# Performance work log

Hardware: AMD Instinct MI355X
Metric: run time of the kernel (lower is better)

The kernel has to match this reference:

```python
import jax, jax.numpy as jnp
import numpy as np

B, L, D_IN, D_EXP, N_EXP = 4, 2048, 1024, 1024, 8


def setup_inputs() -> dict:
    key = jax.random.key(0)
    ks = jax.random.split(key, 5)
    s_in = 1.0 / np.sqrt(D_IN)
    x = jax.random.normal(ks[0], (B, L, D_IN), dtype=jnp.float32)
    # per-expert Dense kernels/biases: (n, d_in, d_exp), (n, d_exp)
    We = jax.random.normal(ks[1], (N_EXP, D_IN, D_EXP), dtype=jnp.float32) * s_in
    be = jnp.zeros((N_EXP, D_EXP), dtype=jnp.float32)
    # gating Dense: (d_in, n), (n)
    Wg = jax.random.normal(ks[2], (D_IN, N_EXP), dtype=jnp.float32) * s_in
    bg = jnp.zeros((N_EXP,), dtype=jnp.float32)
    return {"x": x, "We": We, "be": be, "Wg": Wg, "bg": bg}


def reference(x, We, be, Wg, bg):
    # expert outputs: (b, l, n, d_exp) = relu(x @ We[n] + be[n])
    h = jax.nn.relu(jnp.einsum('bld,ndk->blnk', x, We) + be[None, None, :, :])
    # gate: softmax over experts, (b, l, n)
    gate = jax.nn.softmax(jnp.einsum('bld,dn->bln', x, Wg) + bg, axis=-1)
    # gated weighted sum over experts -> (b, l, d_exp)
    return jnp.einsum('bln,blnk->blk', gate, h)
```

## Files before the change

kernel.cpp:

```cpp
#include <hip/hip_runtime.h>
#include <hip/hip_bf16.h>
#include <stdint.h>

#define M_TOT 8192
#define DIN   1024
#define DEXP  1024
#define NEXP  8

#define BM 256
#define BN 128
#define BK 32
#define NT 128
#define KPP 32
#define SLOT_E 16384
#define EXPSZ (DEXP * DIN)

typedef __attribute__((ext_vector_type(8))) short bf16x8;
typedef __attribute__((ext_vector_type(16))) float f32x16;
typedef __attribute__((ext_vector_type(8))) unsigned short us8;

typedef __attribute__((address_space(1))) void* as1vp;
typedef __attribute__((address_space(3))) void* as3vp;

__device__ __forceinline__ unsigned short f2bf(float f) {
    union { float f; unsigned u; } v; v.f = f;
    return (unsigned short)((v.u + 0x7fffu + ((v.u >> 16) & 1u)) >> 16);
}

__device__ __forceinline__ void gl_lds16(const unsigned short* g, unsigned short* l) {
    __builtin_amdgcn_global_load_lds((as1vp)g, (as3vp)l, 16, 0, 0);
}

#define MFMA32(va, vb, vc) __builtin_amdgcn_mfma_f32_32x32x16_bf16(va, vb, vc, 0, 0, 0)

__global__ __launch_bounds__(256) void cvt_x_k(const float* __restrict__ in,
                                               unsigned short* __restrict__ out, int n8) {
    int i = blockIdx.x * 256 + threadIdx.x;
    int stride = gridDim.x * 256;
    for (; i < n8; i += stride) {
        const float4* p = (const float4*)in + (size_t)i * 2;
        float4 a = p[0], b = p[1];
        us8 o;
        o[0] = f2bf(a.x); o[1] = f2bf(a.y); o[2] = f2bf(a.z); o[3] = f2bf(a.w);
        o[4] = f2bf(b.x); o[5] = f2bf(b.y); o[6] = f2bf(b.z); o[7] = f2bf(b.w);
        *(us8*)(out + (size_t)i * 8) = o;
    }
}

__global__ __launch_bounds__(256) void cvt_w_k(const float* __restrict__ We,
                                               unsigned short* __restrict__ Wt) {
    __shared__ float tile[64][65];
    int n  = blockIdx.z;
    int k0 = blockIdx.y * 64;
    int j0 = blockIdx.x * 64;
    int t  = threadIdx.x;
    int tr = t >> 6, tc = t & 63;
    const float* src = We + (size_t)n * DIN * DEXP;
    #pragma unroll
    for (int rr = 0; rr < 16; ++rr) {
        int r = rr * 4 + tr;
        tile[r][tc] = src[(size_t)(k0 + r) * DEXP + j0 + tc];
    }
    __syncthreads();
    unsigned short* dst = Wt + (size_t)n * DEXP * DIN;
    #pragma unroll
    for (int rr = 0; rr < 16; ++rr) {
        int r = rr * 4 + tr;
        dst[(size_t)(j0 + r) * DIN + k0 + tc] = f2bf(tile[tc][r]);
    }
}

__global__ __launch_bounds__(256) void gate_k(const float* __restrict__ x,
                                              const float* __restrict__ Wg,
                                              const float* __restrict__ bg,
                                              float* __restrict__ gate) {
    __shared__ float wgt[NEXP][DIN];
    int t = threadIdx.x;
    for (int idx = t; idx < DIN * NEXP; idx += 256)
        wgt[idx & 7][idx >> 3] = Wg[idx];
    __syncthreads();
    int wid = t >> 6, lane = t & 63;
    for (int m = blockIdx.x * 4 + wid; m < M_TOT; m += gridDim.x * 4) {
        const float* xr = x + (size_t)m * DIN;
        float acc[NEXP];
        #pragma unroll
        for (int n = 0; n < NEXP; ++n) acc[n] = 0.f;
        for (int i = 0; i < DIN / 64; ++i) {
            int d = i * 64 + lane;
            float xv = xr[d];
            #pragma unroll
            for (int n = 0; n < NEXP; ++n) acc[n] = fmaf(xv, wgt[n][d], acc[n]);
        }
        #pragma unroll
        for (int n = 0; n < NEXP; ++n) {
            #pragma unroll
            for (int off = 32; off; off >>= 1) acc[n] += __shfl_xor(acc[n], off);
            acc[n] += bg[n];
        }
        float mx = acc[0];
        #pragma unroll
        for (int n = 1; n < NEXP; ++n) mx = fmaxf(mx, acc[n]);
        float s = 0.f, e[NEXP];
        #pragma unroll
        for (int n = 0; n < NEXP; ++n) { e[n] = __expf(acc[n] - mx); s += e[n]; }
        float inv = 1.f / s;
        if (lane < NEXP) gate[(size_t)m * NEXP + lane] = e[lane] * inv;
    }
}

__global__ __launch_bounds__(512, 2) void moe_k(const unsigned short* __restrict__ Xb,
                                                const unsigned short* __restrict__ Wt,
                                                const float* __restrict__ gate,
                                                const float* __restrict__ be,
                                                float* __restrict__ out) {
    __shared__ __align__(16) unsigned short lds[4 * SLOT_E];
    __shared__ float gateL[BM * NEXP];
    __shared__ float biasL[NEXP * BN];

    const int t    = threadIdx.x;
    const int lane = t & 63;
    const int wv   = t >> 6;
    const int wm   = wv >> 1;
    const int wn   = wv & 1;
    const int l31  = lane & 31;
    const int lhi  = lane >> 5;

    const int b    = blockIdx.x;
    const int lg   = (b & 7) * 32 + (b >> 3);
    const int brow = (lg >> 3) * BM;
    const int bcol = (lg & 7) * BN;

    const int sA = (t >> 2) * DIN + ((((t & 3) - (t >> 3)) & 3) * 8);
    const unsigned short* gA = Xb + (size_t)brow * DIN;
    const unsigned short* gB = Wt + (size_t)bcol * DIN;

    const int kc0 = ((lhi + (l31 >> 1)) & 3) * 8;
    const int kc1 = kc0 ^ 16;
    const int aOff0 = (wm * 64 + l31) * 32 + kc0;
    const int aOff1 = (wm * 64 + l31) * 32 + kc1;
    const int bOff0 = 8192 + (wn * 64 + l31) * 32 + kc0;
    const int bOff1 = 8192 + (wn * 64 + l31) * 32 + kc1;

#define STAGE_A(sl_, k0_) do { \
    const unsigned short* g_ = gA + (k0_) + sA; \
    unsigned short* d_ = (unsigned short*)lds + (sl_) * SLOT_E + t * 8; \
    gl_lds16(g_, d_); gl_lds16(g_ + 128 * DIN, d_ + 4096); } while (0)
#define STAGE_B0(sl_, e_, k0_) do { \
    gl_lds16(gB + (size_t)(e_) * EXPSZ + (k0_) + sA, \
             (unsigned short*)lds + (sl_) * SLOT_E + 8192 + t * 8); } while (0)
#define STAGE_B1(sl_, e_, k0_) do { \
    gl_lds16(gB + (size_t)(e_) * EXPSZ + (k0_) + sA, \
             (unsigned short*)lds + (sl_) * SLOT_E + 12288 + t * 8); } while (0)

#define RD_B0(L_) do { \
    b0[0][0] = *(const bf16x8*)((L_) + bOff0); \
    b0[0][1] = *(const bf16x8*)((L_) + bOff1); \
    b0[1][0] = *(const bf16x8*)((L_) + bOff0 + 1024); \
    b0[1][1] = *(const bf16x8*)((L_) + bOff1 + 1024); } while (0)
#define RD_A(L_) do { \
    a[0][0] = *(const bf16x8*)((L_) + aOff0); \
    a[0][1] = *(const bf16x8*)((L_) + aOff1); \
    a[1][0] = *(const bf16x8*)((L_) + aOff0 + 1024); \
    a[1][1] = *(const bf16x8*)((L_) + aOff1 + 1024); } while (0)
#define RD_B1(L_) do { \
    b1[0][0] = *(const bf16x8*)((L_) + bOff0 + 4096); \
    b1[0][1] = *(const bf16x8*)((L_) + bOff1 + 4096); \
    b1[1][0] = *(const bf16x8*)((L_) + bOff0 + 5120); \
    b1[1][1] = *(const bf16x8*)((L_) + bOff1 + 5120); } while (0)

    f32x16 acc_e0[2][2] = {};
    f32x16 acc_e1[2][2] = {};
    f32x16 acc_o[2][2]  = {};
    bf16x8 a[2][2], b0[2][2], b1[2][2];

    {
        const float* gp = gate + (size_t)brow * NEXP;
        ((float4*)gateL)[t] = ((const float4*)gp)[t];
        if (t < 256)
            ((float4*)biasL)[t] =
                *(const float4*)(be + (size_t)(t >> 5) * DEXP + bcol + (t & 31) * 4);
    }
    STAGE_A(0, 0);  STAGE_B0(0, 0, 0);  STAGE_B1(0, 1, 0);
    STAGE_A(1, 32); STAGE_B0(1, 0, 32); STAGE_B1(1, 1, 32);
    STAGE_A(2, 64); STAGE_B0(2, 0, 64); STAGE_B1(2, 1, 64);
    asm volatile("s_waitcnt vmcnt(4)" ::: "memory");
    asm volatile("s_waitcnt lgkmcnt(0)" ::: "memory");
    __builtin_amdgcn_s_barrier();
    RD_B0(lds); RD_A(lds);
    __builtin_amdgcn_sched_barrier(0);
    RD_B1(lds);
    __builtin_amdgcn_sched_barrier(0);

    for (int T = 0; T < NT; ++T) {
        asm volatile("s_waitcnt lgkmcnt(4)" ::: "memory");
        __builtin_amdgcn_sched_barrier(0);
        __builtin_amdgcn_s_setprio(1);
        #pragma unroll
        for (int mf = 0; mf < 2; ++mf)
            #pragma unroll
            for (int nf = 0; nf < 2; ++nf) {
                acc_e0[mf][nf] = MFMA32(a[mf][0], b0[nf][0], acc_e0[mf][nf]);
                acc_e0[mf][nf] = MFMA32(a[mf][1], b0[nf][1], acc_e0[mf][nf]);
            }
        __builtin_amdgcn_s_setprio(0);

        if (T < NT - 1) {
            const unsigned short* L1 = lds + ((T + 1) & 3) * SLOT_E;
            RD_B0(L1);
            asm volatile("s_waitcnt lgkmcnt(4)" ::: "memory");
        } else {
            asm volatile("s_waitcnt lgkmcnt(0)" ::: "memory");
        }
        __builtin_amdgcn_sched_barrier(0);
        __builtin_amdgcn_s_setprio(1);
        #pragma unroll
        for (int mf = 0; mf < 2; ++mf)
            #pragma unroll
            for (int nf = 0; nf < 2; ++nf) {
                acc_e1[mf][nf] = MFMA32(a[mf][0], b1[nf][0], acc_e1[mf][nf]);
                acc_e1[mf][nf] = MFMA32(a[mf][1], b1[nf][1], acc_e1[mf][nf]);
            }
        __builtin_amdgcn_s_setprio(0);

        if ((T & (KPP - 1)) == (KPP - 1)) {
            const int e0 = (T >> 5) * 2, e1 = e0 + 1;
            float bi0[2], bi1[2];
            #pragma unroll
            for (int nf = 0; nf < 2; ++nf) {
                bi0[nf] = biasL[e0 * BN + wn * 64 + nf * 32 + l31];
                bi1[nf] = biasL[e1 * BN + wn * 64 + nf * 32 + l31];
            }
            #pragma unroll
            for (int mf = 0; mf < 2; ++mf) {
                #pragma unroll
                for (int reg = 0; reg < 16; ++reg) {
                    const int rl = wm * 64 + mf * 32 + (reg & 3) + 8 * (reg >> 2) + 4 * lhi;
                    const float g0 = gateL[rl * NEXP + e0];
                    const float g1 = gateL[rl * NEXP + e1];
                    #pragma unroll
                    for (int nf = 0; nf < 2; ++nf) {
                        acc_o[mf][nf][reg] += g0 * fmaxf(acc_e0[mf][nf][reg] + bi0[nf], 0.f)
                                            + g1 * fmaxf(acc_e1[mf][nf][reg] + bi1[nf], 0.f);
                    }
                }
            }
            #pragma unroll
            for (int mf = 0; mf < 2; ++mf)
                #pragma unroll
                for (int nf = 0; nf < 2; ++nf) {
                    acc_e0[mf][nf] = (f32x16){};
                    acc_e1[mf][nf] = (f32x16){};
                }
        }

        if (T < NT - 1) {
            const unsigned short* L1 = lds + ((T + 1) & 3) * SLOT_E;
            RD_A(L1);
            __builtin_amdgcn_sched_barrier(0);
            RD_B1(L1);
            __builtin_amdgcn_sched_barrier(0);
        }

        if (T < NT - 3) {
            const int s3 = (T + 3) & 3;
            const int e3 = ((T + 3) >> 5) * 2;
            const int k3 = ((T + 3) & (KPP - 1)) * BK;
            STAGE_A(s3, k3); STAGE_B0(s3, e3, k3); STAGE_B1(s3, e3 + 1, k3);
            asm volatile("s_waitcnt vmcnt(4)" ::: "memory");
        } else {
            asm volatile("s_waitcnt vmcnt(0)" ::: "memory");
        }
        __builtin_amdgcn_s_barrier();
    }

    #pragma unroll
    for (int mf = 0; mf < 2; ++mf) {
        #pragma unroll
        for (int reg = 0; reg < 16; ++reg) {
            const int rl = wm * 64 + mf * 32 + (reg & 3) + 8 * (reg >> 2) + 4 * lhi;
            float* op = out + (size_t)(brow + rl) * DEXP + bcol + wn * 64 + l31;
            #pragma unroll
            for (int nf = 0; nf < 2; ++nf) op[nf * 32] = acc_o[mf][nf][reg];
        }
    }
#undef STAGE_A
#undef STAGE_B0
#undef STAGE_B1
#undef RD_A
#undef RD_B0
#undef RD_B1
}

extern "C" void kernel_launch(void* const* d_in, const int* in_sizes, int n_in,
                              void* d_out, int out_size, void* d_ws, size_t ws_size,
                              hipStream_t stream) {
    const float* x  = (const float*)d_in[0];
    const float* We = (const float*)d_in[1];
    const float* be = (const float*)d_in[2];
    const float* Wg = (const float*)d_in[3];
    const float* bg = (const float*)d_in[4];
    float* out = (float*)d_out;

    unsigned short* Xb = (unsigned short*)d_ws;
    unsigned short* Wt = Xb + (size_t)M_TOT * DIN;
    float* gate = (float*)(Wt + (size_t)NEXP * DEXP * DIN);

    hipLaunchKernelGGL(cvt_x_k, dim3(2048), dim3(256), 0, stream, x, Xb, M_TOT * DIN / 8);
    hipLaunchKernelGGL(cvt_w_k, dim3(16, 16, 8), dim3(256), 0, stream, We, Wt);
    hipLaunchKernelGGL(gate_k, dim3(512), dim3(256), 0, stream, x, Wg, bg, gate);
    hipLaunchKernelGGL(moe_k, dim3((M_TOT / BM) * (DEXP / BN)), dim3(512), 0, stream,
                       Xb, Wt, gate, be, out);
}
```

Measured before the change: 159.8 us.

## Fuse x bf16 conversion into gate kernel and double-buffer A fragments in MoE loop

Removes the separate x-to-bf16 kernel and does the conversion inside the gating kernel, which already reads each row of x. This saves one launch and one full read of x. In the main MFMA loop, A fragments are now double-buffered in registers (aX/aY) and the loop is unrolled by two. The next A and B0 fragments are read from LDS right after the first MFMA group rather than after the epilogue, to overlap LDS reads with compute. This costs more VGPRs and changes the lgkmcnt wait thresholds, which could hurt occupancy or scheduling.

Result: slower. 351.5 us (+119.9%).

```diff
diff --git a/kernel.cpp b/kernel.cpp
--- a/kernel.cpp
+++ b/kernel.cpp
@@ -32,20 +32,6 @@
 }
 
 #define MFMA32(va, vb, vc) __builtin_amdgcn_mfma_f32_32x32x16_bf16(va, vb, vc, 0, 0, 0)
-
-__global__ __launch_bounds__(256) void cvt_x_k(const float* __restrict__ in,
-                                               unsigned short* __restrict__ out, int n8) {
-    int i = blockIdx.x * 256 + threadIdx.x;
-    int stride = gridDim.x * 256;
-    for (; i < n8; i += stride) {
-        const float4* p = (const float4*)in + (size_t)i * 2;
-        float4 a = p[0], b = p[1];
-        us8 o;
-        o[0] = f2bf(a.x); o[1] = f2bf(a.y); o[2] = f2bf(a.z); o[3] = f2bf(a.w);
-        o[4] = f2bf(b.x); o[5] = f2bf(b.y); o[6] = f2bf(b.z); o[7] = f2bf(b.w);
-        *(us8*)(out + (size_t)i * 8) = o;
-    }
-}
 
 __global__ __launch_bounds__(256) void cvt_w_k(const float* __restrict__ We,
                                                unsigned short* __restrict__ Wt) {
@@ -70,10 +56,11 @@
     }
 }
 
-__global__ __launch_bounds__(256) void gate_k(const float* __restrict__ x,
-                                              const float* __restrict__ Wg,
-                                              const float* __restrict__ bg,
-                                              float* __restrict__ gate) {
+__global__ __launch_bounds__(256) void gatex_k(const float* __restrict__ x,
+                                               const float* __restrict__ Wg,
+                                               const float* __restrict__ bg,
+                                               float* __restrict__ gate,
+                                               unsigned short* __restrict__ Xb) {
     __shared__ float wgt[NEXP][DIN];
     int t = threadIdx.x;
     for (int idx = t; idx < DIN * NEXP; idx += 256)
@@ -82,6 +69,17 @@
     int wid = t >> 6, lane = t & 63;
     for (int m = blockIdx.x * 4 + wid; m < M_TOT; m += gridDim.x * 4) {
         const float* xr = x + (size_t)m * DIN;
+        unsigned short* xb = Xb + (size_t)m * DIN;
+        #pragma unroll
+        for (int p = 0; p < 2; ++p) {
+            int d = p * 512 + lane * 8;
+            float4 v0 = *(const float4*)(xr + d);
+            float4 v1 = *(const float4*)(xr + d + 4);
+            us8 o;
+            o[0] = f2bf(v0.x); o[1] = f2bf(v0.y); o[2] = f2bf(v0.z); o[3] = f2bf(v0.w);
+            o[4] = f2bf(v1.x); o[5] = f2bf(v1.y); o[6] = f2bf(v1.z); o[7] = f2bf(v1.w);
+            *(us8*)(xb + d) = o;
+        }
         float acc[NEXP];
         #pragma unroll
         for (int n = 0; n < NEXP; ++n) acc[n] = 0.f;
@@ -157,11 +155,11 @@
     b0[0][1] = *(const bf16x8*)((L_) + bOff1); \
     b0[1][0] = *(const bf16x8*)((L_) + bOff0 + 1024); \
     b0[1][1] = *(const bf16x8*)((L_) + bOff1 + 1024); } while (0)
-#define RD_A(L_) do { \
-    a[0][0] = *(const bf16x8*)((L_) + aOff0); \
-    a[0][1] = *(const bf16x8*)((L_) + aOff1); \
-    a[1][0] = *(const bf16x8*)((L_) + aOff0 + 1024); \
-    a[1][1] = *(const bf16x8*)((L_) + aOff1 + 1024); } while (0)
+#define RD_AS(S_, L_) do { \
+    S_[0][0] = *(const bf16x8*)((L_) + aOff0); \
+    S_[0][1] = *(const bf16x8*)((L_) + aOff1); \
+    S_[1][0] = *(const bf16x8*)((L_) + aOff0 + 1024); \
+    S_[1][1] = *(const bf16x8*)((L_) + aOff1 + 1024); } while (0)
 #define RD_B1(L_) do { \
     b1[0][0] = *(const bf16x8*)((L_) + bOff0 + 4096); \
     b1[0][1] = *(const bf16x8*)((L_) + bOff1 + 4096); \
@@ -171,7 +169,7 @@
     f32x16 acc_e0[2][2] = {};
     f32x16 acc_e1[2][2] = {};
     f32x16 acc_o[2][2]  = {};
-    bf16x8 a[2][2], b0[2][2], b1[2][2];
+    bf16x8 aX[2][2], aY[2][2], b0[2][2], b1[2][2];
 
     {
         const float* gp = gate + (size_t)brow * NEXP;
@@ -186,91 +184,93 @@
     asm volatile("s_waitcnt vmcnt(4)" ::: "memory");
     asm volatile("s_waitcnt lgkmcnt(0)" ::: "memory");
     __builtin_amdgcn_s_barrier();
-    RD_B0(lds); RD_A(lds);
+    RD_B0(lds);
+    __builtin_amdgcn_sched_barrier(0);
+    RD_AS(aX, lds);
     __builtin_amdgcn_sched_barrier(0);
     RD_B1(lds);
     __builtin_amdgcn_sched_barrier(0);
 
-    for (int T = 0; T < NT; ++T) {
-        asm volatile("s_waitcnt lgkmcnt(4)" ::: "memory");
-        __builtin_amdgcn_sched_barrier(0);
-        __builtin_amdgcn_s_setprio(1);
-        #pragma unroll
-        for (int mf = 0; mf < 2; ++mf)
-            #pragma unroll
-            for (int nf = 0; nf < 2; ++nf) {
-                acc_e0[mf][nf] = MFMA32(a[mf][0], b0[nf][0], acc_e0[mf][nf]);
-                acc_e0[mf][nf] = MFMA32(a[mf][1], b0[nf][1], acc_e0[mf][nf]);
-            }
-        __builtin_amdgcn_s_setprio(0);
-
-        if (T < NT - 1) {
-            const unsigned short* L1 = lds + ((T + 1) & 3) * SLOT_E;
-            RD_B0(L1);
-            asm volatile("s_waitcnt lgkmcnt(4)" ::: "memory");
-        } else {
-            asm volatile("s_waitcnt lgkmcnt(0)" ::: "memory");
-        }
-        __builtin_amdgcn_sched_barrier(0);
-        __builtin_amdgcn_s_setprio(1);
-        #pragma unroll
-        for (int mf = 0; mf < 2; ++mf)
-            #pragma unroll
-            for (int nf = 0; nf < 2; ++nf) {
-                acc_e1[mf][nf] = MFMA32(a[mf][0], b1[nf][0], acc_e1[mf][nf]);
-                acc_e1[mf][nf] = MFMA32(a[mf][1], b1[nf][1], acc_e1[mf][nf]);
-            }
-        __builtin_amdgcn_s_setprio(0);
-
-        if ((T & (KPP - 1)) == (KPP - 1)) {
-            const int e0 = (T >> 5) * 2, e1 = e0 + 1;
-            float bi0[2], bi1[2];
-            #pragma unroll
-            for (int nf = 0; nf < 2; ++nf) {
-                bi0[nf] = biasL[e0 * BN + wn * 64 + nf * 32 + l31];
-                bi1[nf] = biasL[e1 * BN + wn * 64 + nf * 32 + l31];
-            }
-            #pragma unroll
-            for (int mf = 0; mf < 2; ++mf) {
-                #pragma unroll
-                for (int reg = 0; reg < 16; ++reg) {
-                    const int rl = wm * 64 + mf * 32 + (reg & 3) + 8 * (reg >> 2) + 4 * lhi;
-                    const float g0 = gateL[rl * NEXP + e0];
-                    const float g1 = gateL[rl * NEXP + e1];
-                    #pragma unroll
-                    for (int nf = 0; nf < 2; ++nf) {
-                        acc_o[mf][nf][reg] += g0 * fmaxf(acc_e0[mf][nf][reg] + bi0[nf], 0.f)
-                                            + g1 * fmaxf(acc_e1[mf][nf][reg] + bi1[nf], 0.f);
-                    }
-                }
-            }
-            #pragma unroll
-            for (int mf = 0; mf < 2; ++mf)
-                #pragma unroll
-                for (int nf = 0; nf < 2; ++nf) {
-                    acc_e0[mf][nf] = (f32x16){};
-                    acc_e1[mf][nf] = (f32x16){};
-                }
-        }
-
-        if (T < NT - 1) {
-            const unsigned short* L1 = lds + ((T + 1) & 3) * SLOT_E;
-            RD_A(L1);
-            __builtin_amdgcn_sched_barrier(0);
-            RD_B1(L1);
-            __builtin_amdgcn_sched_barrier(0);
-        }
-
-        if (T < NT - 3) {
-            const int s3 = (T + 3) & 3;
-            const int e3 = ((T + 3) >> 5) * 2;
-            const int k3 = ((T + 3) & (KPP - 1)) * BK;
-            STAGE_A(s3, k3); STAGE_B0(s3, e3, k3); STAGE_B1(s3, e3 + 1, k3);
-            asm volatile("s_waitcnt vmcnt(4)" ::: "memory");
-        } else {
-            asm volatile("s_waitcnt vmcnt(0)" ::: "memory");
-        }
-        __builtin_amdgcn_s_barrier();
+#define EPILOGUE(pg_) do { \
+    const int e0_ = (pg_) * 2, e1_ = e0_ + 1; \
+    float bi0[2], bi1[2]; \
+    _Pragma("unroll") \
+    for (int nf = 0; nf < 2; ++nf) { \
+        bi0[nf] = biasL[e0_ * BN + wn * 64 + nf * 32 + l31]; \
+        bi1[nf] = biasL[e1_ * BN + wn * 64 + nf * 32 + l31]; \
+    } \
+    _Pragma("unroll") \
+    for (int mf = 0; mf < 2; ++mf) { \
+        _Pragma("unroll") \
+        for (int reg = 0; reg < 16; ++reg) { \
+            const int rl_ = wm * 64 + mf * 32 + (reg & 3) + 8 * (reg >> 2) + 4 * lhi; \
+            const float g0_ = gateL[rl_ * NEXP + e0_]; \
+            const float g1_ = gateL[rl_ * NEXP + e1_]; \
+            _Pragma("unroll") \
+            for (int nf = 0; nf < 2; ++nf) { \
+                acc_o[mf][nf][reg] += g0_ * fmaxf(acc_e0[mf][nf][reg] + bi0[nf], 0.f) \
+                                    + g1_ * fmaxf(acc_e1[mf][nf][reg] + bi1[nf], 0.f); \
+            } \
+        } \
+    } \
+    _Pragma("unroll") \
+    for (int mf = 0; mf < 2; ++mf) \
+        _Pragma("unroll") \
+        for (int nf = 0; nf < 2; ++nf) { \
+            acc_e0[mf][nf] = (f32x16){}; \
+            acc_e1[mf][nf] = (f32x16){}; \
+        } } while (0)
+
+#define ITER(T_, AC, AN, DO_EPI) do { \
+    const unsigned short* L1_ = lds + (((T_) + 1) & 3) * SLOT_E; \
+    asm volatile("s_waitcnt lgkmcnt(4)" ::: "memory"); \
+    __builtin_amdgcn_sched_barrier(0); \
+    __builtin_amdgcn_s_setprio(1); \
+    _Pragma("unroll") \
+    for (int mf = 0; mf < 2; ++mf) \
+        _Pragma("unroll") \
+        for (int nf = 0; nf < 2; ++nf) { \
+            acc_e0[mf][nf] = MFMA32(AC[mf][0], b0[nf][0], acc_e0[mf][nf]); \
+            acc_e0[mf][nf] = MFMA32(AC[mf][1], b0[nf][1], acc_e0[mf][nf]); \
+        } \
+    __builtin_amdgcn_s_setprio(0); \
+    __builtin_amdgcn_sched_barrier(0); \
+    if ((T_) < NT - 1) { \
+        RD_B0(L1_); \
+        __builtin_amdgcn_sched_barrier(0); \
+        RD_AS(AN, L1_); \
+        __builtin_amdgcn_sched_barrier(0); \
+        asm volatile("s_waitcnt lgkmcnt(8)" ::: "memory"); \
+    } else { \
+        asm volatile("s_waitcnt lgkmcnt(0)" ::: "memory"); \
+    } \
+    __builtin_amdgcn_sched_barrier(0); \
+    __builtin_amdgcn_s_setprio(1); \
+    _Pragma("unroll") \
+    for (int mf = 0; mf < 2; ++mf) \
+        _Pragma("unroll") \
+        for (int nf = 0; nf < 2; ++nf) { \
+            acc_e1[mf][nf] = MFMA32(AC[mf][0], b1[nf][0], acc_e1[mf][nf]); \
+            acc_e1[mf][nf] = MFMA32(AC[mf][1], b1[nf][1], acc_e1[mf][nf]); \
+        } \
+    __builtin_amdgcn_s_setprio(0); \
+    __builtin_amdgcn_sched_barrier(0); \
+    if ((T_) < NT - 1) { RD_B1(L1_); __builtin_amdgcn_sched_barrier(0); } \
+    if (DO_EPI && (((T_) & (KPP - 1)) == (KPP - 1))) EPILOGUE((T_) >> 5); \
+    if ((T_) < NT - 3) { \
+        const int s3_ = ((T_) + 3) & 3; \
+        const int e3_ = (((T_) + 3) >> 5) * 2; \
+        const int k3_ = (((T_) + 3) & (KPP - 1)) * BK; \
+        STAGE_A(s3_, k3_); STAGE_B0(s3_, e3_, k3_); STAGE_B1(s3_, e3_ + 1, k3_); \
+        asm volatile("s_waitcnt vmcnt(4)" ::: "memory"); \
+    } else { \
+        asm volatile("s_waitcnt vmcnt(0)" ::: "memory"); \
+    } \
+    __builtin_amdgcn_s_barrier(); } while (0)
+
+    for (int T = 0; T < NT; T += 2) {
+        ITER(T,     aX, aY, 0);
+        ITER(T + 1, aY, aX, 1);
     }
 
     #pragma unroll
@@ -286,9 +286,11 @@
 #undef STAGE_A
 #undef STAGE_B0
 #undef STAGE_B1
-#undef RD_A
+#undef RD_AS
 #undef RD_B0
 #undef RD_B1
+#undef ITER
+#undef EPILOGUE
 }
 
 extern "C" void kernel_launch(void* const* d_in, const int* in_sizes, int n_in,
@@ -305,9 +307,8 @@
     unsigned short* Wt = Xb + (size_t)M_TOT * DIN;
     float* gate = (float*)(Wt + (size_t)NEXP * DEXP * DIN);
 
-    hipLaunchKernelGGL(cvt_x_k, dim3(2048), dim3(256), 0, stream, x, Xb, M_TOT * DIN / 8);
     hipLaunchKernelGGL(cvt_w_k, dim3(16, 16, 8), dim3(256), 0, stream, We, Wt);
-    hipLaunchKernelGGL(gate_k, dim3(512), dim3(256), 0, stream, x, Wg, bg, gate);
+    hipLaunchKernelGGL(gatex_k, dim3(512), dim3(256), 0, stream, x, Wg, bg, gate, Xb);
     hipLaunchKernelGGL(moe_k, dim3((M_TOT / BM) * (DEXP / BN)), dim3(512), 0, stream,
                        Xb, Wt, gate, be, out);
 }
```

## Shrink MoE GEMM tile to 128x128 with 3-stage LDS ring and fuse x conversion into gating

Applied to the files above, without the earlier changes.

Fuses the fp32-to-bf16 conversion of x into the gating kernel, so x is read once for both jobs and one launch is dropped. The main MoE GEMM tile shrinks from 256x128 with 512 threads to 128x128 with 256 threads. The LDS ring drops from 4 slots to 3, with the slot index and vmcnt waits adjusted to match. The grid doubles, which should give more blocks per CU and better wave balance, at the cost of lower arithmetic intensity per block and more weight re-reads.

After: 180.5 us. 1.13x slower.

```diff
diff --git a/kernel.cpp b/kernel.cpp
--- a/kernel.cpp
+++ b/kernel.cpp
@@ -7,12 +7,12 @@
 #define DEXP  1024
 #define NEXP  8
 
-#define BM 256
+#define BM 128
 #define BN 128
 #define BK 32
 #define NT 128
 #define KPP 32
-#define SLOT_E 16384
+#define SLOT_E 12288
 #define EXPSZ (DEXP * DIN)
 
 typedef __attribute__((ext_vector_type(8))) short bf16x8;
@@ -32,20 +32,6 @@
 }
 
 #define MFMA32(va, vb, vc) __builtin_amdgcn_mfma_f32_32x32x16_bf16(va, vb, vc, 0, 0, 0)
-
-__global__ __launch_bounds__(256) void cvt_x_k(const float* __restrict__ in,
-                                               unsigned short* __restrict__ out, int n8) {
-    int i = blockIdx.x * 256 + threadIdx.x;
-    int stride = gridDim.x * 256;
-    for (; i < n8; i += stride) {
-        const float4* p = (const float4*)in + (size_t)i * 2;
-        float4 a = p[0], b = p[1];
-        us8 o;
-        o[0] = f2bf(a.x); o[1] = f2bf(a.y); o[2] = f2bf(a.z); o[3] = f2bf(a.w);
-        o[4] = f2bf(b.x); o[5] = f2bf(b.y); o[6] = f2bf(b.z); o[7] = f2bf(b.w);
-        *(us8*)(out + (size_t)i * 8) = o;
-    }
-}
 
 __global__ __launch_bounds__(256) void cvt_w_k(const float* __restrict__ We,
                                                unsigned short* __restrict__ Wt) {
@@ -70,10 +56,11 @@
     }
 }
 
-__global__ __launch_bounds__(256) void gate_k(const float* __restrict__ x,
-                                              const float* __restrict__ Wg,
-                                              const float* __restrict__ bg,
-                                              float* __restrict__ gate) {
+__global__ __launch_bounds__(256) void gatex_k(const float* __restrict__ x,
+                                               const float* __restrict__ Wg,
+                                               const float* __restrict__ bg,
+                                               float* __restrict__ gate,
+                                               unsigned short* __restrict__ Xb) {
     __shared__ float wgt[NEXP][DIN];
     int t = threadIdx.x;
     for (int idx = t; idx < DIN * NEXP; idx += 256)
@@ -82,6 +69,17 @@
     int wid = t >> 6, lane = t & 63;
     for (int m = blockIdx.x * 4 + wid; m < M_TOT; m += gridDim.x * 4) {
         const float* xr = x + (size_t)m * DIN;
+        unsigned short* xb = Xb + (size_t)m * DIN;
+        #pragma unroll
+        for (int p = 0; p < 2; ++p) {
+            int d = p * 512 + lane * 8;
+            float4 v0 = *(const float4*)(xr + d);
+            float4 v1 = *(const float4*)(xr + d + 4);
+            us8 o;
+            o[0] = f2bf(v0.x); o[1] = f2bf(v0.y); o[2] = f2bf(v0.z); o[3] = f2bf(v0.w);
+            o[4] = f2bf(v1.x); o[5] = f2bf(v1.y); o[6] = f2bf(v1.z); o[7] = f2bf(v1.w);
+            *(us8*)(xb + d) = o;
+        }
         float acc[NEXP];
         #pragma unroll
         for (int n = 0; n < NEXP; ++n) acc[n] = 0.f;
@@ -108,12 +106,12 @@
     }
 }
 
-__global__ __launch_bounds__(512, 2) void moe_k(const unsigned short* __restrict__ Xb,
+__global__ __launch_bounds__(256, 2) void moe_k(const unsigned short* __restrict__ Xb,
                                                 const unsigned short* __restrict__ Wt,
                                                 const float* __restrict__ gate,
                                                 const float* __restrict__ be,
                                                 float* __restrict__ out) {
-    __shared__ __align__(16) unsigned short lds[4 * SLOT_E];
+    __shared__ __align__(16) unsigned short lds[3 * SLOT_E];
     __shared__ float gateL[BM * NEXP];
     __shared__ float biasL[NEXP * BN];
 
@@ -126,7 +124,7 @@
     const int lhi  = lane >> 5;
 
     const int b    = blockIdx.x;
-    const int lg   = (b & 7) * 32 + (b >> 3);
+    const int lg   = (b & 7) * 64 + (b >> 3);
     const int brow = (lg >> 3) * BM;
     const int bcol = (lg & 7) * BN;
 
@@ -138,19 +136,21 @@
     const int kc1 = kc0 ^ 16;
     const int aOff0 = (wm * 64 + l31) * 32 + kc0;
     const int aOff1 = (wm * 64 + l31) * 32 + kc1;
-    const int bOff0 = 8192 + (wn * 64 + l31) * 32 + kc0;
-    const int bOff1 = 8192 + (wn * 64 + l31) * 32 + kc1;
+    const int bOff0 = 4096 + (wn * 64 + l31) * 32 + kc0;
+    const int bOff1 = 4096 + (wn * 64 + l31) * 32 + kc1;
 
 #define STAGE_A(sl_, k0_) do { \
     const unsigned short* g_ = gA + (k0_) + sA; \
     unsigned short* d_ = (unsigned short*)lds + (sl_) * SLOT_E + t * 8; \
-    gl_lds16(g_, d_); gl_lds16(g_ + 128 * DIN, d_ + 4096); } while (0)
+    gl_lds16(g_, d_); gl_lds16(g_ + 64 * DIN, d_ + 2048); } while (0)
 #define STAGE_B0(sl_, e_, k0_) do { \
-    gl_lds16(gB + (size_t)(e_) * EXPSZ + (k0_) + sA, \
-             (unsigned short*)lds + (sl_) * SLOT_E + 8192 + t * 8); } while (0)
+    const unsigned short* g_ = gB + (size_t)(e_) * EXPSZ + (k0_) + sA; \
+    unsigned short* d_ = (unsigned short*)lds + (sl_) * SLOT_E + 4096 + t * 8; \
+    gl_lds16(g_, d_); gl_lds16(g_ + 64 * DIN, d_ + 2048); } while (0)
 #define STAGE_B1(sl_, e_, k0_) do { \
-    gl_lds16(gB + (size_t)(e_) * EXPSZ + (k0_) + sA, \
-             (unsigned short*)lds + (sl_) * SLOT_E + 12288 + t * 8); } while (0)
+    const unsigned short* g_ = gB + (size_t)(e_) * EXPSZ + (k0_) + sA; \
+    unsigned short* d_ = (unsigned short*)lds + (sl_) * SLOT_E + 8192 + t * 8; \
+    gl_lds16(g_, d_); gl_lds16(g_ + 64 * DIN, d_ + 2048); } while (0)
 
 #define RD_B0(L_) do { \
     b0[0][0] = *(const bf16x8*)((L_) + bOff0); \
@@ -176,14 +176,13 @@
     {
         const float* gp = gate + (size_t)brow * NEXP;
         ((float4*)gateL)[t] = ((const float4*)gp)[t];
-        if (t < 256)
-            ((float4*)biasL)[t] =
-                *(const float4*)(be + (size_t)(t >> 5) * DEXP + bcol + (t & 31) * 4);
+        ((float4*)biasL)[t] =
+            *(const float4*)(be + (size_t)(t >> 5) * DEXP + bcol + (t & 31) * 4);
     }
     STAGE_A(0, 0);  STAGE_B0(0, 0, 0);  STAGE_B1(0, 1, 0);
     STAGE_A(1, 32); STAGE_B0(1, 0, 32); STAGE_B1(1, 1, 32);
     STAGE_A(2, 64); STAGE_B0(2, 0, 64); STAGE_B1(2, 1, 64);
-    asm volatile("s_waitcnt vmcnt(4)" ::: "memory");
+    asm volatile("s_waitcnt vmcnt(12)" ::: "memory");
     asm volatile("s_waitcnt lgkmcnt(0)" ::: "memory");
     __builtin_amdgcn_s_barrier();
     RD_B0(lds); RD_A(lds);
@@ -191,7 +190,10 @@
     RD_B1(lds);
     __builtin_amdgcn_sched_barrier(0);
 
+    int sl = 0;
     for (int T = 0; T < NT; ++T) {
+        const unsigned short* L1 = lds + ((sl == 2) ? 0 : sl + 1) * SLOT_E;
+
         asm volatile("s_waitcnt lgkmcnt(4)" ::: "memory");
         __builtin_amdgcn_sched_barrier(0);
         __builtin_amdgcn_s_setprio(1);
@@ -205,7 +207,6 @@
         __builtin_amdgcn_s_setprio(0);
 
         if (T < NT - 1) {
-            const unsigned short* L1 = lds + ((T + 1) & 3) * SLOT_E;
             RD_B0(L1);
             asm volatile("s_waitcnt lgkmcnt(4)" ::: "memory");
         } else {
@@ -254,7 +255,6 @@
         }
 
         if (T < NT - 1) {
-            const unsigned short* L1 = lds + ((T + 1) & 3) * SLOT_E;
             RD_A(L1);
             __builtin_amdgcn_sched_barrier(0);
             RD_B1(L1);
@@ -262,15 +262,17 @@
         }
 
         if (T < NT - 3) {
-            const int s3 = (T + 3) & 3;
+            const int s3 = (T + 3) % 3;
             const int e3 = ((T + 3) >> 5) * 2;
             const int k3 = ((T + 3) & (KPP - 1)) * BK;
             STAGE_A(s3, k3); STAGE_B0(s3, e3, k3); STAGE_B1(s3, e3 + 1, k3);
-            asm volatile("s_waitcnt vmcnt(4)" ::: "memory");
+            asm volatile("s_waitcnt vmcnt(6)" ::: "memory");
         } else {
             asm volatile("s_waitcnt vmcnt(0)" ::: "memory");
         }
         __builtin_amdgcn_s_barrier();
+
+        sl = (sl == 2) ? 0 : sl + 1;
     }
 
     #pragma unroll
@@ -305,9 +307,8 @@
     unsigned short* Wt = Xb + (size_t)M_TOT * DIN;
     float* gate = (float*)(Wt + (size_t)NEXP * DEXP * DIN);
 
-    hipLaunchKernelGGL(cvt_x_k, dim3(2048), dim3(256), 0, stream, x, Xb, M_TOT * DIN / 8);
     hipLaunchKernelGGL(cvt_w_k, dim3(16, 16, 8), dim3(256), 0, stream, We, Wt);
-    hipLaunchKernelGGL(gate_k, dim3(512), dim3(256), 0, stream, x, Wg, bg, gate);
-    hipLaunchKernelGGL(moe_k, dim3((M_TOT / BM) * (DEXP / BN)), dim3(512), 0, stream,
+    hipLaunchKernelGGL(gatex_k, dim3(512), dim3(256), 0, stream, x, Wg, bg, gate, Xb);
+    hipLaunchKernelGGL(moe_k, dim3((M_TOT / BM) * (DEXP / BN)), dim3(256), 0, stream,
                        Xb, Wt, gate, be, out);
 }
```
